# Performance work log

Measured on AMD Instinct MI355X. Metric: run time of the kernel, lower is better.

Reference implementation:

```python
import jax, jax.numpy as jnp
import numpy as np

GROUP_SIZE = 128


def _dequant_groupwise(values, scales, group_size):
    # values: [rows, cols] int codes; scales: [rows, cols//group_size]
    rows, cols = values.shape
    groups = cols // group_size  # dims chosen to divide evenly (no padding branch)
    v = values.astype(jnp.float32).reshape(rows, groups, group_size)
    return (v * scales[:, :, None]).reshape(rows, cols)


def setup_inputs() -> dict:
    key = jax.random.key(0)
    ks = jax.random.split(key, 8)
    tokens, d_in, d_out, rank = 8192, 4096, 4096, 256
    return {
        "x": jax.random.normal(ks[0], (tokens, d_in), dtype=jnp.float32),
        "q_values": jax.random.randint(ks[1], (d_out, d_in), 0, 16, dtype=jnp.int32),
        "q_scales": jax.random.uniform(ks[2], (d_out, d_in // GROUP_SIZE), dtype=jnp.float32),
        "l_values": jax.random.randint(ks[3], (d_out, rank), 0, 16, dtype=jnp.int32),
        "l_scales": jax.random.uniform(ks[4], (d_out, rank // GROUP_SIZE), dtype=jnp.float32),
        "r_values": jax.random.randint(ks[5], (rank, d_in), 0, 16, dtype=jnp.int32),
        "r_scales": jax.random.uniform(ks[6], (rank, d_in // GROUP_SIZE), dtype=jnp.float32),
        "bias": jax.random.normal(ks[7], (d_out,), dtype=jnp.float32),
    }


def reference(x, q_values, q_scales, l_values, l_scales, r_values, r_scales, bias):
    # Dequantize groupwise int-quantized weights, then y = x @ Q^T + (x @ R^T) @ L^T + b
    q = _dequant_groupwise(q_values, q_scales, GROUP_SIZE)  # [out, in]
    l = _dequant_groupwise(l_values, l_scales, GROUP_SIZE)  # [out, rank]
    r = _dequant_groupwise(r_values, r_scales, GROUP_SIZE)  # [rank, in]
    xr = jnp.einsum('ti,ri->tr', x, r)          # [tokens, rank]
    base = jnp.einsum('ti,oi->to', x, q)        # [tokens, out]
    low_rank = jnp.einsum('tr,or->to', xr, l)   # [tokens, out]
    return base + low_rank + bias
```

## Files before the change

kernel.cpp:

```cpp
#include <hip/hip_runtime.h>
#include <cstdint>
#include <cstddef>

#define BM 128
#define BN 128
#define BK 64

typedef float f32x4 __attribute__((ext_vector_type(4)));
typedef __bf16 bf16x8 __attribute__((ext_vector_type(8)));

__device__ __forceinline__ unsigned short f2bf(float f) {
    unsigned int u = __float_as_uint(f);
    u += 0x7fffu + ((u >> 16) & 1u);
    return (unsigned short)(u >> 16);
}

__device__ __forceinline__ void async_copy16(const void* g, void* l) {
    __builtin_amdgcn_global_load_lds(
        (__attribute__((address_space(1))) void*)(g),
        (__attribute__((address_space(3))) void*)(l), 16, 0, 0);
}


__global__ void cast_x_kernel(const float* __restrict__ x,
                              unsigned short* __restrict__ o, int n8) {
    int i = blockIdx.x * blockDim.x + threadIdx.x;
    if (i >= n8) return;
    const float4* xv = (const float4*)x;
    float4 a = xv[2 * (size_t)i];
    float4 b = xv[2 * (size_t)i + 1];
    union { unsigned short u[8]; uint4 v; } r;
    r.u[0] = f2bf(a.x); r.u[1] = f2bf(a.y); r.u[2] = f2bf(a.z); r.u[3] = f2bf(a.w);
    r.u[4] = f2bf(b.x); r.u[5] = f2bf(b.y); r.u[6] = f2bf(b.z); r.u[7] = f2bf(b.w);
    ((uint4*)o)[i] = r.v;
}

__global__ void dequant_kernel(const int* __restrict__ v,
                               const float* __restrict__ s,
                               unsigned short* __restrict__ o,
                               int colshift, int gpr, int n8) {
    int i = blockIdx.x * blockDim.x + threadIdx.x;
    if (i >= n8) return;
    int e = i * 8;
    int row = e >> colshift;
    int col = e & ((1 << colshift) - 1);
    float sc = s[row * gpr + (col >> 7)];
    int4 a = ((const int4*)v)[2 * (size_t)i];
    int4 b = ((const int4*)v)[2 * (size_t)i + 1];
    union { unsigned short u[8]; uint4 x; } r;
    r.u[0] = f2bf(a.x * sc); r.u[1] = f2bf(a.y * sc);
    r.u[2] = f2bf(a.z * sc); r.u[3] = f2bf(a.w * sc);
    r.u[4] = f2bf(b.x * sc); r.u[5] = f2bf(b.y * sc);
    r.u[6] = f2bf(b.z * sc); r.u[7] = f2bf(b.w * sc);
    ((uint4*)o)[i] = r.x;
}

__global__ void __launch_bounds__(256)
gemm_bt_kernel(const __bf16* __restrict__ A1, int lda1, int k1steps,
               const __bf16* __restrict__ B1,
               const __bf16* __restrict__ A2, int lda2, int k2steps,
               const __bf16* __restrict__ B2,
               const float* __restrict__ bias,
               float* __restrict__ outf,
               unsigned short* __restrict__ outb,
               int ldo) {
    __shared__ __bf16 As[BM * BK];
    __shared__ __bf16 Bs[BN * BK];

    const int tid  = threadIdx.x;
    const int lane = tid & 63;
    const int wave = tid >> 6;
    const int wm = (wave >> 1) * 64;
    const int wn = (wave & 1) * 64;
    const int mBase = blockIdx.y * BM;
    const int nBase = blockIdx.x * BN;
    const int lrow = lane >> 3;
    const int lcol = (((lane & 7) ^ lrow) & 7) * 8;

    f32x4 acc[4][4] = {};

    #pragma unroll 1
    for (int phase = 0; phase < 2; ++phase) {
        const __bf16* A = phase ? A2 : A1;
        const __bf16* B = phase ? B2 : B1;
        const int lda    = phase ? lda2 : lda1;
        const int ksteps = phase ? k2steps : k1steps;

        for (int kt = 0; kt < ksteps; ++kt) {
            const int k0 = kt * BK;
            #pragma unroll
            for (int r = 0; r < 4; ++r) {
                const int chunk = wave * 4 + r;
                const int row = chunk * 8 + lrow;
                async_copy16(A + (size_t)(mBase + row) * lda + (k0 + lcol),
                             &As[chunk * 512]);
                async_copy16(B + (size_t)(nBase + row) * lda + (k0 + lcol),
                             &Bs[chunk * 512]);
            }
            __syncthreads();

            #pragma unroll
            for (int ks = 0; ks < 2; ++ks) {
                const int kofs = ks * 32 + (lane >> 4) * 8;
                const int swz = kofs >> 3;
                bf16x8 af[4], bfr[4];
                #pragma unroll
                for (int i = 0; i < 4; ++i) {
                    const int m = wm + i * 16 + (lane & 15);
                    af[i] = *(const bf16x8*)&As[m * BK + (((swz ^ m) & 7) << 3)];
                }
                #pragma unroll
                for (int j = 0; j < 4; ++j) {
                    const int n = wn + j * 16 + (lane & 15);
                    bfr[j] = *(const bf16x8*)&Bs[n * BK + (((swz ^ n) & 7) << 3)];
                }
                #pragma unroll
                for (int i = 0; i < 4; ++i)
                    #pragma unroll
                    for (int j = 0; j < 4; ++j)
                        acc[i][j] = __builtin_amdgcn_mfma_f32_16x16x32_bf16(
                            af[i], bfr[j], acc[i][j], 0, 0, 0);
            }
            __syncthreads();
        }
    }

    const int cn = lane & 15;
    const int rg = (lane >> 4) * 4;
    if (outf) {
        #pragma unroll
        for (int j = 0; j < 4; ++j) {
            const int o = nBase + wn + j * 16 + cn;
            const float bv = bias[o];
            #pragma unroll
            for (int i = 0; i < 4; ++i) {
                const int t0 = mBase + wm + i * 16 + rg;
                #pragma unroll
                for (int r = 0; r < 4; ++r)
                    outf[(size_t)(t0 + r) * ldo + o] = acc[i][j][r] + bv;
            }
        }
    } else {
        #pragma unroll
        for (int j = 0; j < 4; ++j) {
            const int o = nBase + wn + j * 16 + cn;
            #pragma unroll
            for (int i = 0; i < 4; ++i) {
                const int t0 = mBase + wm + i * 16 + rg;
                #pragma unroll
                for (int r = 0; r < 4; ++r)
                    outb[(size_t)(t0 + r) * ldo + o] = f2bf(acc[i][j][r]);
            }
        }
    }
}

extern "C" void kernel_launch(void* const* d_in, const int* in_sizes, int n_in,
                              void* d_out, int out_size, void* d_ws, size_t ws_size,
                              hipStream_t stream) {
    const float* x    = (const float*)d_in[0];
    const int*   qv   = (const int*)d_in[1];
    const float* qs   = (const float*)d_in[2];
    const int*   lv   = (const int*)d_in[3];
    const float* ls   = (const float*)d_in[4];
    const int*   rv   = (const int*)d_in[5];
    const float* rs   = (const float*)d_in[6];
    const float* bias = (const float*)d_in[7];
    float* out = (float*)d_out;

    const int T = 8192, DI = 4096, DO = 4096, R = 256;

    char* ws = (char*)d_ws;
    unsigned short* xb = (unsigned short*)(ws);
    unsigned short* Qd = (unsigned short*)(ws + 67108864);
    unsigned short* Rd = (unsigned short*)(ws + 100663296);
    unsigned short* Ld = (unsigned short*)(ws + 102760448);
    unsigned short* xr = (unsigned short*)(ws + 104857600);

    {
        int n8 = T * DI / 8;
        cast_x_kernel<<<(n8 + 255) / 256, 256, 0, stream>>>(x, xb, n8);
    }
    {
        int n8 = DO * DI / 8;
        dequant_kernel<<<(n8 + 255) / 256, 256, 0, stream>>>(qv, qs, Qd, 12, DI / 128, n8);
    }
    {
        int n8 = DO * R / 8;
        dequant_kernel<<<(n8 + 255) / 256, 256, 0, stream>>>(lv, ls, Ld, 8, R / 128, n8);
    }
    {
        int n8 = R * DI / 8;
        dequant_kernel<<<(n8 + 255) / 256, 256, 0, stream>>>(rv, rs, Rd, 12, DI / 128, n8);
    }
    {
        dim3 g(R / BN, T / BM);
        gemm_bt_kernel<<<g, 256, 0, stream>>>(
            (const __bf16*)xb, DI, DI / BK, (const __bf16*)Rd,
            nullptr, 0, 0, nullptr,
            nullptr, nullptr, xr, R);
    }
    {
        dim3 g(DO / BN, T / BM);
        gemm_bt_kernel<<<g, 256, 0, stream>>>(
            (const __bf16*)xb, DI, DI / BK, (const __bf16*)Qd,
            (const __bf16*)xr, R, R / BK, (const __bf16*)Ld,
            bias, out, nullptr, DO);
    }
}
```

Baseline: 652.7 us.

## Fold low-rank adapter into dequantized weight before the main GEMM

Computes the effective weight W = Q + L·R once (a 4096x4096x256 GEMM whose epilogue adds the dequantized Q), then runs a single x·W^T GEMM. This replaces the separate x·R^T GEMM and the extra K=256 phase over 8192 tokens, and folds the small prep kernels into one launch. R is dequantized into a transposed layout with scattered 2-byte stores. Rounding L·R+Q to bf16 before the multiply changes numerics slightly.

New measurement: 712.4 us. +9.1%, slower.

```diff
diff --git a/kernel.cpp b/kernel.cpp
--- a/kernel.cpp
+++ b/kernel.cpp
@@ -21,46 +21,54 @@
         (__attribute__((address_space(3))) void*)(l), 16, 0, 0);
 }
 
-
-__global__ void cast_x_kernel(const float* __restrict__ x,
-                              unsigned short* __restrict__ o, int n8) {
-    int i = blockIdx.x * blockDim.x + threadIdx.x;
-    if (i >= n8) return;
-    const float4* xv = (const float4*)x;
-    float4 a = xv[2 * (size_t)i];
-    float4 b = xv[2 * (size_t)i + 1];
-    union { unsigned short u[8]; uint4 v; } r;
-    r.u[0] = f2bf(a.x); r.u[1] = f2bf(a.y); r.u[2] = f2bf(a.z); r.u[3] = f2bf(a.w);
-    r.u[4] = f2bf(b.x); r.u[5] = f2bf(b.y); r.u[6] = f2bf(b.z); r.u[7] = f2bf(b.w);
-    ((uint4*)o)[i] = r.v;
-}
-
-__global__ void dequant_kernel(const int* __restrict__ v,
-                               const float* __restrict__ s,
-                               unsigned short* __restrict__ o,
-                               int colshift, int gpr, int n8) {
-    int i = blockIdx.x * blockDim.x + threadIdx.x;
-    if (i >= n8) return;
-    int e = i * 8;
-    int row = e >> colshift;
-    int col = e & ((1 << colshift) - 1);
-    float sc = s[row * gpr + (col >> 7)];
-    int4 a = ((const int4*)v)[2 * (size_t)i];
-    int4 b = ((const int4*)v)[2 * (size_t)i + 1];
-    union { unsigned short u[8]; uint4 x; } r;
-    r.u[0] = f2bf(a.x * sc); r.u[1] = f2bf(a.y * sc);
-    r.u[2] = f2bf(a.z * sc); r.u[3] = f2bf(a.w * sc);
-    r.u[4] = f2bf(b.x * sc); r.u[5] = f2bf(b.y * sc);
-    r.u[6] = f2bf(b.z * sc); r.u[7] = f2bf(b.w * sc);
-    ((uint4*)o)[i] = r.x;
+__global__ void prep_kernel(const float* __restrict__ x, unsigned short* __restrict__ xb,
+                            const int* __restrict__ lv, const float* __restrict__ ls,
+                            unsigned short* __restrict__ Ld,
+                            const int* __restrict__ rv, const float* __restrict__ rs,
+                            unsigned short* __restrict__ RdT,
+                            int NX, int NL, int NR) {
+    int u = blockIdx.x * blockDim.x + threadIdx.x;
+    if (u < NX) {
+        const float4* xv = (const float4*)x;
+        float4 a = xv[2 * (size_t)u];
+        float4 b = xv[2 * (size_t)u + 1];
+        union { unsigned short s[8]; uint4 v; } r;
+        r.s[0] = f2bf(a.x); r.s[1] = f2bf(a.y); r.s[2] = f2bf(a.z); r.s[3] = f2bf(a.w);
+        r.s[4] = f2bf(b.x); r.s[5] = f2bf(b.y); r.s[6] = f2bf(b.z); r.s[7] = f2bf(b.w);
+        ((uint4*)xb)[u] = r.v;
+    } else if (u < NX + NL) {
+        int i = u - NX;
+        int e = i * 8;
+        int row = e >> 8, col = e & 255;
+        float sc = ls[row * 2 + (col >> 7)];
+        int4 a = ((const int4*)lv)[2 * (size_t)i];
+        int4 b = ((const int4*)lv)[2 * (size_t)i + 1];
+        union { unsigned short s[8]; uint4 v; } r;
+        r.s[0] = f2bf(a.x * sc); r.s[1] = f2bf(a.y * sc);
+        r.s[2] = f2bf(a.z * sc); r.s[3] = f2bf(a.w * sc);
+        r.s[4] = f2bf(b.x * sc); r.s[5] = f2bf(b.y * sc);
+        r.s[6] = f2bf(b.z * sc); r.s[7] = f2bf(b.w * sc);
+        ((uint4*)Ld)[i] = r.v;
+    } else if (u < NX + NL + NR) {
+        int i = u - NX - NL;
+        int e = i * 8;
+        int row = e >> 12, col = e & 4095;
+        float sc = rs[row * 32 + (col >> 7)];
+        int4 a = ((const int4*)rv)[2 * (size_t)i];
+        int4 b = ((const int4*)rv)[2 * (size_t)i + 1];
+        int c[8] = {a.x, a.y, a.z, a.w, b.x, b.y, b.z, b.w};
+        #pragma unroll
+        for (int j = 0; j < 8; ++j)
+            RdT[(size_t)(col + j) * 256 + row] = f2bf(c[j] * sc);
+    }
 }
 
 __global__ void __launch_bounds__(256)
-gemm_bt_kernel(const __bf16* __restrict__ A1, int lda1, int k1steps,
-               const __bf16* __restrict__ B1,
-               const __bf16* __restrict__ A2, int lda2, int k2steps,
-               const __bf16* __restrict__ B2,
+gemm_bt_kernel(const __bf16* __restrict__ A, int lda, int ksteps,
+               const __bf16* __restrict__ B,
                const float* __restrict__ bias,
+               const int* __restrict__ qv,
+               const float* __restrict__ qsc,
                float* __restrict__ outf,
                unsigned short* __restrict__ outb,
                int ldo) {
@@ -79,50 +87,42 @@
 
     f32x4 acc[4][4] = {};
 
-    #pragma unroll 1
-    for (int phase = 0; phase < 2; ++phase) {
-        const __bf16* A = phase ? A2 : A1;
-        const __bf16* B = phase ? B2 : B1;
-        const int lda    = phase ? lda2 : lda1;
-        const int ksteps = phase ? k2steps : k1steps;
-
-        for (int kt = 0; kt < ksteps; ++kt) {
-            const int k0 = kt * BK;
-            #pragma unroll
-            for (int r = 0; r < 4; ++r) {
-                const int chunk = wave * 4 + r;
-                const int row = chunk * 8 + lrow;
-                async_copy16(A + (size_t)(mBase + row) * lda + (k0 + lcol),
-                             &As[chunk * 512]);
-                async_copy16(B + (size_t)(nBase + row) * lda + (k0 + lcol),
-                             &Bs[chunk * 512]);
-            }
-            __syncthreads();
-
-            #pragma unroll
-            for (int ks = 0; ks < 2; ++ks) {
-                const int kofs = ks * 32 + (lane >> 4) * 8;
-                const int swz = kofs >> 3;
-                bf16x8 af[4], bfr[4];
+    for (int kt = 0; kt < ksteps; ++kt) {
+        const int k0 = kt * BK;
+        #pragma unroll
+        for (int r = 0; r < 4; ++r) {
+            const int chunk = wave * 4 + r;
+            const int row = chunk * 8 + lrow;
+            async_copy16(A + (size_t)(mBase + row) * lda + (k0 + lcol),
+                         &As[chunk * 512]);
+            async_copy16(B + (size_t)(nBase + row) * lda + (k0 + lcol),
+                         &Bs[chunk * 512]);
+        }
+        __syncthreads();
+
+        #pragma unroll
+        for (int ks = 0; ks < 2; ++ks) {
+            const int kofs = ks * 32 + (lane >> 4) * 8;
+            const int swz = kofs >> 3;
+            bf16x8 af[4], bfr[4];
+            #pragma unroll
+            for (int i = 0; i < 4; ++i) {
+                const int m = wm + i * 16 + (lane & 15);
+                af[i] = *(const bf16x8*)&As[m * BK + (((swz ^ m) & 7) << 3)];
+            }
+            #pragma unroll
+            for (int j = 0; j < 4; ++j) {
+                const int n = wn + j * 16 + (lane & 15);
+                bfr[j] = *(const bf16x8*)&Bs[n * BK + (((swz ^ n) & 7) << 3)];
+            }
+            #pragma unroll
+            for (int i = 0; i < 4; ++i)
                 #pragma unroll
-                for (int i = 0; i < 4; ++i) {
-                    const int m = wm + i * 16 + (lane & 15);
-                    af[i] = *(const bf16x8*)&As[m * BK + (((swz ^ m) & 7) << 3)];
-                }
-                #pragma unroll
-                for (int j = 0; j < 4; ++j) {
-                    const int n = wn + j * 16 + (lane & 15);
-                    bfr[j] = *(const bf16x8*)&Bs[n * BK + (((swz ^ n) & 7) << 3)];
-                }
-                #pragma unroll
-                for (int i = 0; i < 4; ++i)
-                    #pragma unroll
-                    for (int j = 0; j < 4; ++j)
-                        acc[i][j] = __builtin_amdgcn_mfma_f32_16x16x32_bf16(
-                            af[i], bfr[j], acc[i][j], 0, 0, 0);
-            }
-            __syncthreads();
-        }
+                for (int j = 0; j < 4; ++j)
+                    acc[i][j] = __builtin_amdgcn_mfma_f32_16x16x32_bf16(
+                        af[i], bfr[j], acc[i][j], 0, 0, 0);
+        }
+        __syncthreads();
     }
 
     const int cn = lane & 15;
@@ -141,6 +141,7 @@
             }
         }
     } else {
+        const int sld = ldo >> 7;
         #pragma unroll
         for (int j = 0; j < 4; ++j) {
             const int o = nBase + wn + j * 16 + cn;
@@ -148,8 +149,13 @@
             for (int i = 0; i < 4; ++i) {
                 const int t0 = mBase + wm + i * 16 + rg;
                 #pragma unroll
-                for (int r = 0; r < 4; ++r)
-                    outb[(size_t)(t0 + r) * ldo + o] = f2bf(acc[i][j][r]);
+                for (int r = 0; r < 4; ++r) {
+                    float v = acc[i][j][r];
+                    if (qv)
+                        v += (float)qv[(size_t)(t0 + r) * ldo + o] *
+                             qsc[(size_t)(t0 + r) * sld + (o >> 7)];
+                    outb[(size_t)(t0 + r) * ldo + o] = f2bf(v);
+                }
             }
         }
     }
@@ -171,40 +177,27 @@
     const int T = 8192, DI = 4096, DO = 4096, R = 256;
 
     char* ws = (char*)d_ws;
-    unsigned short* xb = (unsigned short*)(ws);
-    unsigned short* Qd = (unsigned short*)(ws + 67108864);
-    unsigned short* Rd = (unsigned short*)(ws + 100663296);
-    unsigned short* Ld = (unsigned short*)(ws + 102760448);
-    unsigned short* xr = (unsigned short*)(ws + 104857600);
+    unsigned short* xb  = (unsigned short*)(ws);
+    unsigned short* Wd  = (unsigned short*)(ws + 67108864);
+    unsigned short* Ld  = (unsigned short*)(ws + 100663296);
+    unsigned short* RdT = (unsigned short*)(ws + 102760448);
 
     {
-        int n8 = T * DI / 8;
-        cast_x_kernel<<<(n8 + 255) / 256, 256, 0, stream>>>(x, xb, n8);
+        int NX = T * DI / 8, NL = DO * R / 8, NR = R * DI / 8;
+        int n = NX + NL + NR;
+        prep_kernel<<<(n + 255) / 256, 256, 0, stream>>>(
+            x, xb, lv, ls, Ld, rv, rs, RdT, NX, NL, NR);
     }
     {
-        int n8 = DO * DI / 8;
-        dequant_kernel<<<(n8 + 255) / 256, 256, 0, stream>>>(qv, qs, Qd, 12, DI / 128, n8);
-    }
-    {
-        int n8 = DO * R / 8;
-        dequant_kernel<<<(n8 + 255) / 256, 256, 0, stream>>>(lv, ls, Ld, 8, R / 128, n8);
-    }
-    {
-        int n8 = R * DI / 8;
-        dequant_kernel<<<(n8 + 255) / 256, 256, 0, stream>>>(rv, rs, Rd, 12, DI / 128, n8);
-    }
-    {
-        dim3 g(R / BN, T / BM);
+        dim3 g(DI / BN, DO / BM);
         gemm_bt_kernel<<<g, 256, 0, stream>>>(
-            (const __bf16*)xb, DI, DI / BK, (const __bf16*)Rd,
-            nullptr, 0, 0, nullptr,
-            nullptr, nullptr, xr, R);
+            (const __bf16*)Ld, R, R / BK, (const __bf16*)RdT,
+            nullptr, qv, qs, nullptr, Wd, DI);
     }
     {
         dim3 g(DO / BN, T / BM);
         gemm_bt_kernel<<<g, 256, 0, stream>>>(
-            (const __bf16*)xb, DI, DI / BK, (const __bf16*)Qd,
-            (const __bf16*)xr, R, R / BK, (const __bf16*)Ld,
-            bias, out, nullptr, DO);
-    }
-}
+            (const __bf16*)xb, DI, DI / BK, (const __bf16*)Wd,
+            bias, nullptr, nullptr, out, nullptr, DO);
+    }
+}
```
